# Optimization experiments

Hardware: AMD Instinct MI355X
Metric: run time of the kernel (lower is better)

## Reference

```python
import jax, jax.numpy as jnp
import numpy as np


def setup_inputs() -> dict:
    key = jax.random.key(0)
    k = jax.random.split(key, 8)
    n, C, L = 16, 32, 128
    dim, out_c, n_pieces = 256, 128, 20
    x = jax.random.normal(k[0], (n, C, L), dtype=jnp.float32)
    mask = jnp.ones((n, L), dtype=jnp.float32)
    # conv1: Conv2d(2C+2, dim, 1) -> weight [dim, 2C+2]
    fan1 = 2 * C + 2
    w1 = jax.random.normal(k[1], (dim, fan1), dtype=jnp.float32) / np.sqrt(fan1)
    b1 = jnp.zeros((dim,), dtype=jnp.float32)
    # conv2: Conv2d(dim, out_c, 1) -> weight [out_c, dim]
    w2 = jax.random.normal(k[2], (out_c, dim), dtype=jnp.float32) / np.sqrt(dim)
    b2 = jnp.zeros((out_c,), dtype=jnp.float32)
    # FSPool weight: [out_c, n_pieces+1], init normal_
    pool_w = jax.random.normal(k[3], (out_c, n_pieces + 1), dtype=jnp.float32)
    return {"x": x, "mask": mask, "w1": w1, "b1": b1, "w2": w2, "b2": b2, "pool_w": pool_w}


def reference(x, mask, w1, b1, w2, b2, pool_w):
    # x: [n, C, L], mask: [n, L]
    xm = jnp.concatenate([x, mask[:, None, :]], axis=1)  # [n, C+1, L]
    c1 = xm.shape[1]
    # conv1 on concat([a_expand, b_expand], dim=1) with a 1x1 conv factors:
    # W1 @ cat(a,b) = W1a @ a + W1b @ b, avoiding the [n, 2C+2, L, L] tensor.
    ha = jnp.einsum('dc,ncl->ndl', w1[:, :c1], xm)  # [n, dim, L] (row part)
    hb = jnp.einsum('dc,ncl->ndl', w1[:, c1:], xm)  # [n, dim, L] (col part)
    h = jax.nn.relu(ha[:, :, :, None] + hb[:, :, None, :] + b1[None, :, None, None])  # [n, dim, L, L]
    y = jnp.einsum('od,ndij->noij', w2, h) + b2[None, :, None, None]  # [n, out_c, L, L]
    n, oc, L, _ = y.shape
    L2 = L * L
    y = y.reshape(n, oc, L2) / L2  # x / l / l
    # FSPool: all set sizes equal L2, so the size mask is all-ones (the -99999
    # masking and (1-mask) terms are no-ops).
    n_pieces = pool_w.shape[1] - 1
    pos = jnp.minimum(jnp.arange(L2, dtype=jnp.float32) / max(L2 - 1, 1), 1.0)  # [L2]
    idx_f = n_pieces * pos
    idx = idx_f.astype(jnp.int32)
    frac = idx_f - idx.astype(jnp.float32)
    left = pool_w[:, idx]                                  # [oc, L2]
    right = pool_w[:, jnp.minimum(idx + 1, n_pieces)]      # [oc, L2]
    w = (1.0 - frac)[None, :] * left + frac[None, :] * right  # [oc, L2]
    y_sorted = -jnp.sort(-y, axis=2)  # descending sort along set dim
    pooled = jnp.sum(y_sorted * w[None, :, :], axis=2)  # [n, oc]
    return pooled
```

## Files before the change

kernel.cpp:

```cpp
#include <hip/hip_runtime.h>
#include <hip/hip_bf16.h>


#define NB 16
#define CIN 33
#define DIM 256
#define LEN 128
#define OC 128
#define L2 16384

typedef short bf16x8 __attribute__((ext_vector_type(8)));
typedef float f32x4 __attribute__((ext_vector_type(4)));

__device__ __forceinline__ unsigned short f32_to_bf16_rne(float f) {
    unsigned u = __float_as_uint(f);
    unsigned rb = ((u >> 16) & 1u) + 0x7FFFu;
    return (unsigned short)((u + rb) >> 16);
}
__device__ __forceinline__ float bf16_to_f32(unsigned short b) {
    return __uint_as_float(((unsigned)b) << 16);
}
__device__ __forceinline__ unsigned pk_bf16(float a, float b) {
    __hip_bfloat162 p = __float22bfloat162_rn(make_float2(a, b));
    unsigned w;
    __builtin_memcpy(&w, &p, 4);
    return w;
}

__global__ __launch_bounds__(128) void kA(const float* __restrict__ x,
                                          const float* __restrict__ mask,
                                          const float* __restrict__ w1,
                                          const float* __restrict__ b1,
                                          float* __restrict__ ha,
                                          float* __restrict__ hb) {
    int d = blockIdx.x;
    int n = blockIdx.y;
    int l = threadIdx.x;
    const float* w1r = w1 + d * (2 * CIN);
    float a = 0.f, b = 0.f;
#pragma unroll
    for (int c = 0; c < CIN; ++c) {
        float xv = (c < 32) ? x[((size_t)n * 32 + c) * LEN + l] : mask[(size_t)n * LEN + l];
        a = fmaf(w1r[c], xv, a);
        b = fmaf(w1r[CIN + c], xv, b);
    }
    float hb1 = 0.5f * b1[d];
    ha[((size_t)n * DIM + d) * LEN + l] = a + hb1;
    hb[((size_t)n * DIM + d) * LEN + l] = b + hb1;
}

__global__ __launch_bounds__(256) void kW(const float* __restrict__ w2,
                                          unsigned short* __restrict__ w2h) {
    int idx = blockIdx.x * 256 + threadIdx.x;
    w2h[idx] = f32_to_bf16_rne(w2[idx]);
}

#define ROWP 40
__global__ __launch_bounds__(256) void kB(const float* __restrict__ ha,
                                          const float* __restrict__ hb,
                                          const unsigned short* __restrict__ w2h,
                                          const float* __restrict__ b2,
                                          unsigned short* __restrict__ y,
                                          int nbase) {
    __shared__ unsigned short Bh[128 * ROWP];
    __shared__ float ha_s[DIM];
    int i0 = blockIdx.x;
    int zloc = blockIdx.y;
    int n = nbase + zloc;
    int tid = threadIdx.x;
    int wv = tid >> 6, l = tid & 63;
    int g = l >> 4, lr = l & 15;

    if (tid < DIM) ha_s[tid] = ha[((size_t)n * DIM + tid) * LEN + i0];

    f32x4 acc[2][8];
#pragma unroll
    for (int mt = 0; mt < 2; ++mt) {
        float bv[4];
#pragma unroll
        for (int r = 0; r < 4; ++r) bv[r] = b2[(wv * 2 + mt) * 16 + g * 4 + r];
#pragma unroll
        for (int nt = 0; nt < 8; ++nt)
#pragma unroll
            for (int r = 0; r < 4; ++r) acc[mt][nt][r] = bv[r];
    }

    const float* hbN = hb + (size_t)n * DIM * LEN;
    int j = tid & 127, kh = tid >> 7;
    __syncthreads();

    for (int d0 = 0; d0 < DIM; d0 += 32) {
        {
            union { unsigned w[8]; uint4 q[2]; } pkv;
#pragma unroll
            for (int kk = 0; kk < 16; kk += 2) {
                int d = d0 + kh * 16 + kk;
                float h0 = fmaxf(ha_s[d] + hbN[(size_t)d * LEN + j], 0.f);
                float h1 = fmaxf(ha_s[d + 1] + hbN[(size_t)(d + 1) * LEN + j], 0.f);
                pkv.w[kk >> 1] = pk_bf16(h0, h1);
            }
            *(uint4*)&Bh[j * ROWP + kh * 16] = pkv.q[0];
            *(uint4*)&Bh[j * ROWP + kh * 16 + 8] = pkv.q[1];
        }
        __syncthreads();

        bf16x8 ah[2];
#pragma unroll
        for (int mt = 0; mt < 2; ++mt) {
            int row = (wv * 2 + mt) * 16 + lr;
            ah[mt] = *(const bf16x8*)&w2h[(size_t)row * DIM + d0 + g * 8];
        }
#pragma unroll
        for (int nt = 0; nt < 8; ++nt) {
            int brow = nt * 16 + lr;
            bf16x8 bh = *(bf16x8*)&Bh[brow * ROWP + g * 8];
#pragma unroll
            for (int mt = 0; mt < 2; ++mt)
                acc[mt][nt] = __builtin_amdgcn_mfma_f32_16x16x32_bf16(ah[mt], bh, acc[mt][nt], 0, 0, 0);
        }
        __syncthreads();
    }

#pragma unroll
    for (int mt = 0; mt < 2; ++mt)
#pragma unroll
        for (int nt = 0; nt < 8; ++nt)
#pragma unroll
            for (int r = 0; r < 4; ++r) {
                int o = (wv * 2 + mt) * 16 + g * 4 + r;
                int col = nt * 16 + lr;
                y[((size_t)zloc * OC + o) * L2 + (size_t)i0 * LEN + col] =
                    f32_to_bf16_rne(acc[mt][nt][r]);
            }
}

__device__ __forceinline__ unsigned swz(unsigned w) { return w ^ ((w >> 2) & 0xCu); }

__global__ __launch_bounds__(1024, 8) void kC(const unsigned short* __restrict__ y,
                                              const float* __restrict__ pw,
                                              float* __restrict__ out,
                                              int nbase) {
    extern __shared__ unsigned hist[];
    int row = blockIdx.x;
    int och = row & (OC - 1);
    int n = nbase + (row >> 7);
    int t = threadIdx.x;
    int lane = t & 63, wv = t >> 6;
    const unsigned short* yr = y + (size_t)row * L2;
    const float* pwo = pw + och * 21;
    float* pwT = (float*)&hist[16384 + 16];
    int tsw = (t & 3) << 2;

#pragma unroll
    for (int q = 0; q < 4; ++q)
        *(uint4*)&hist[t * 16 + ((q << 2) ^ tsw)] = make_uint4(0, 0, 0, 0);
    if (t < 21) pwT[t] = pwo[t];
    if (t == 21) pwT[21] = pwo[20];
    __syncthreads();

    unsigned off16[8];
    {
        union { uint4 q[2]; unsigned short u[16]; } ld;
        ld.q[0] = *(const uint4*)&yr[t * 16];
        ld.q[1] = *(const uint4*)&yr[t * 16 + 8];
#pragma unroll
        for (int e = 0; e < 16; ++e) {
            unsigned u = ld.u[e];
            unsigned k16 = u ^ ((u & 0x8000u) ? 0xFFFFu : 0x8000u);
            unsigned hi = (k16 >> 1) & 1;
            unsigned old = atomicAdd(&hist[swz(k16 >> 2)], hi ? 0x10000u : 1u);
            unsigned myoff = hi ? (old >> 16) : (old & 0xFFFFu);
            if (e & 1) off16[e >> 1] |= myoff << 16;
            else       off16[e >> 1] = myoff;
        }
    }
    __syncthreads();

    int Ti = 0;
#pragma unroll
    for (int q = 0; q < 4; ++q) {
        uint4 v4 = *(const uint4*)&hist[t * 16 + ((q << 2) ^ tsw)];
        Ti += (int)(v4.x & 0xFFFFu) + (int)(v4.x >> 16);
        Ti += (int)(v4.y & 0xFFFFu) + (int)(v4.y >> 16);
        Ti += (int)(v4.z & 0xFFFFu) + (int)(v4.z >> 16);
        Ti += (int)(v4.w & 0xFFFFu) + (int)(v4.w >> 16);
    }
    int incl = Ti;
#pragma unroll
    for (int d = 1; d < 64; d <<= 1) {
        int u2 = __shfl_up(incl, d, 64);
        if (lane >= d) incl += u2;
    }
    if (lane == 63) hist[16384 + wv] = (unsigned)incl;
    __syncthreads();
    int base = 0;
#pragma unroll
    for (int k = 0; k < 16; ++k) {
        int tw = (int)hist[16384 + k];
        base += (k < wv) ? tw : 0;
    }
    int P = base + (incl - Ti);

#pragma unroll
    for (int q = 0; q < 4; ++q) {
        unsigned* wp = &hist[t * 16 + ((q << 2) ^ tsw)];
        uint4 v4 = *(const uint4*)wp;
        unsigned r4[4] = {v4.x, v4.y, v4.z, v4.w};
#pragma unroll
        for (int c = 0; c < 4; ++c) {
            int clo = (int)(r4[c] & 0xFFFFu), chi = (int)(r4[c] >> 16);
            P += clo;
            unsigned slo = (unsigned)(L2 - P);
            P += chi;
            unsigned shi = (unsigned)(L2 - P);
            r4[c] = slo | (shi << 16);
        }
        *(uint4*)wp = make_uint4(r4[0], r4[1], r4[2], r4[3]);
    }
    __syncthreads();

    float acc = 0.f;
    {
        union { uint4 q[2]; unsigned short u[16]; } ld;
        ld.q[0] = *(const uint4*)&yr[t * 16];
        ld.q[1] = *(const uint4*)&yr[t * 16 + 8];
#pragma unroll
        for (int e = 0; e < 16; ++e) {
            unsigned u = ld.u[e];
            unsigned k16 = u ^ ((u & 0x8000u) ? 0xFFFFu : 0x8000u);
            unsigned hi = (k16 >> 1) & 1;
            unsigned w = hist[swz(k16 >> 2)];
            unsigned start = hi ? (w >> 16) : (w & 0xFFFFu);
            unsigned myoff = (e & 1) ? (off16[e >> 1] >> 16) : (off16[e >> 1] & 0xFFFFu);
            int r = (int)(start + myoff);
            float posf = fminf((float)r * (1.0f / 16383.0f), 1.0f);
            float idxf = 20.0f * posf;
            int idx = (int)idxf;
            float frac = idxf - (float)idx;
            float wvw = (1.0f - frac) * pwT[idx] + frac * pwT[idx + 1];
            float val = __uint_as_float(((unsigned)u) << 16);
            acc = fmaf(val, wvw, acc);
        }
    }

#pragma unroll
    for (int d = 32; d >= 1; d >>= 1) acc += __shfl_xor(acc, d, 64);
    __syncthreads();
    if (lane == 0) ((float*)hist)[16384 + wv] = acc;
    __syncthreads();
    if (t == 0) {
        double tot = 0.0;
#pragma unroll
        for (int k = 0; k < 16; ++k) tot += (double)((const float*)hist)[16384 + k];
        out[(size_t)n * OC + och] = (float)(tot * (1.0 / (double)L2));
    }
}

extern "C" void kernel_launch(void* const* d_in, const int* in_sizes, int n_in,
                              void* d_out, int out_size, void* d_ws, size_t ws_size,
                              hipStream_t stream) {
    const float* x    = (const float*)d_in[0];
    const float* mask = (const float*)d_in[1];
    const float* w1   = (const float*)d_in[2];
    const float* b1   = (const float*)d_in[3];
    const float* w2   = (const float*)d_in[4];
    const float* b2   = (const float*)d_in[5];
    const float* pw   = (const float*)d_in[6];
    float* out = (float*)d_out;

    char* ws = (char*)d_ws;
    float* ha = (float*)ws;
    float* hb = ha + (size_t)NB * DIM * LEN;
    unsigned short* w2h = (unsigned short*)(ws + (size_t)2 * NB * DIM * LEN * 4);
    unsigned short* y = w2h + (size_t)2 * OC * DIM;

    size_t used = (size_t)2 * NB * DIM * LEN * 4 + (size_t)2 * OC * DIM * 2;
    size_t perN = (size_t)OC * L2 * 2;
    int nchunk = 1;
    if (ws_size > used + perN) {
        size_t c = (ws_size - used) / perN;
        nchunk = (int)(c > NB ? NB : c);
    }

    hipLaunchKernelGGL(kA, dim3(DIM, NB), dim3(128), 0, stream, x, mask, w1, b1, ha, hb);
    hipLaunchKernelGGL(kW, dim3(OC * DIM / 256), dim3(256), 0, stream, w2, w2h);
    for (int base = 0; base < NB; base += nchunk) {
        int nc = nchunk < (NB - base) ? nchunk : (NB - base);
        hipLaunchKernelGGL(kB, dim3(LEN, nc), dim3(256), 0, stream, ha, hb, w2h, b2, y, base);
        hipLaunchKernelGGL(kC, dim3(OC * nc), dim3(1024), (16384 + 16 + 22) * 4, stream, y, pw, out, base);
    }
}
```

Baseline: 126.7 us.

## Double-buffer the ReLU tile in kB and prefetch the next hb slice during MFMAs

The kB GEMM loop now keeps two shared-memory tiles of the relu(ha+hb) operand. While the current K-slice's MFMAs run, the next slice's hb values are loaded into registers, then converted and written into the other buffer. This hides global load latency behind the matrix ops and cuts one barrier per iteration. The cost is double the shared memory for Bh and 16 more live registers per thread, which could lower occupancy.

Result: no change. 125.2 us (-1.2%).

```diff
diff --git a/kernel.cpp b/kernel.cpp
--- a/kernel.cpp
+++ b/kernel.cpp
@@ -62,7 +62,7 @@
                                           const float* __restrict__ b2,
                                           unsigned short* __restrict__ y,
                                           int nbase) {
-    __shared__ unsigned short Bh[128 * ROWP];
+    __shared__ unsigned short Bh[2][128 * ROWP];
     __shared__ float ha_s[DIM];
     int i0 = blockIdx.x;
     int zloc = blockIdx.y;
@@ -89,21 +89,35 @@
     int j = tid & 127, kh = tid >> 7;
     __syncthreads();
 
-    for (int d0 = 0; d0 < DIM; d0 += 32) {
-        {
-            union { unsigned w[8]; uint4 q[2]; } pkv;
-#pragma unroll
-            for (int kk = 0; kk < 16; kk += 2) {
-                int d = d0 + kh * 16 + kk;
-                float h0 = fmaxf(ha_s[d] + hbN[(size_t)d * LEN + j], 0.f);
-                float h1 = fmaxf(ha_s[d + 1] + hbN[(size_t)(d + 1) * LEN + j], 0.f);
-                pkv.w[kk >> 1] = pk_bf16(h0, h1);
-            }
-            *(uint4*)&Bh[j * ROWP + kh * 16] = pkv.q[0];
-            *(uint4*)&Bh[j * ROWP + kh * 16 + 8] = pkv.q[1];
-        }
-        __syncthreads();
-
+    {
+        float hv[16];
+#pragma unroll
+        for (int kk = 0; kk < 16; ++kk)
+            hv[kk] = hbN[(size_t)(kh * 16 + kk) * LEN + j];
+        union { unsigned w[8]; uint4 q[2]; } pkv;
+#pragma unroll
+        for (int kk = 0; kk < 16; kk += 2) {
+            int d = kh * 16 + kk;
+            pkv.w[kk >> 1] = pk_bf16(fmaxf(ha_s[d] + hv[kk], 0.f),
+                                     fmaxf(ha_s[d + 1] + hv[kk + 1], 0.f));
+        }
+        *(uint4*)&Bh[0][j * ROWP + kh * 16] = pkv.q[0];
+        *(uint4*)&Bh[0][j * ROWP + kh * 16 + 8] = pkv.q[1];
+    }
+    __syncthreads();
+
+#pragma unroll
+    for (int s = 0; s < 8; ++s) {
+        int cur = s & 1;
+        float nv[16];
+        if (s < 7) {
+            int dbase = (s + 1) * 32 + kh * 16;
+#pragma unroll
+            for (int kk = 0; kk < 16; ++kk)
+                nv[kk] = hbN[(size_t)(dbase + kk) * LEN + j];
+        }
+
+        int d0 = s * 32;
         bf16x8 ah[2];
 #pragma unroll
         for (int mt = 0; mt < 2; ++mt) {
@@ -113,10 +127,23 @@
 #pragma unroll
         for (int nt = 0; nt < 8; ++nt) {
             int brow = nt * 16 + lr;
-            bf16x8 bh = *(bf16x8*)&Bh[brow * ROWP + g * 8];
+            bf16x8 bh = *(bf16x8*)&Bh[cur][brow * ROWP + g * 8];
 #pragma unroll
             for (int mt = 0; mt < 2; ++mt)
                 acc[mt][nt] = __builtin_amdgcn_mfma_f32_16x16x32_bf16(ah[mt], bh, acc[mt][nt], 0, 0, 0);
+        }
+
+        if (s < 7) {
+            int dbase = (s + 1) * 32 + kh * 16;
+            union { unsigned w[8]; uint4 q[2]; } pkv;
+#pragma unroll
+            for (int kk = 0; kk < 16; kk += 2) {
+                int d = dbase + kk;
+                pkv.w[kk >> 1] = pk_bf16(fmaxf(ha_s[d] + nv[kk], 0.f),
+                                         fmaxf(ha_s[d + 1] + nv[kk + 1], 0.f));
+            }
+            *(uint4*)&Bh[cur ^ 1][j * ROWP + kh * 16] = pkv.q[0];
+            *(uint4*)&Bh[cur ^ 1][j * ROWP + kh * 16 + 8] = pkv.q[1];
         }
         __syncthreads();
     }
```
